# Optimization experiments

Hardware: AMD Instinct MI355X
Metric: run time of the kernel (lower is better)

The kernel has to match this reference:

```python
import jax, jax.numpy as jnp
import numpy as np

N_POINTS = 300000
N_PAIRS = 100000  # rulebook pairs per kernel offset
K_OFFSETS = 27    # 3x3x3 kernel
C_IN, C_OUT = 32, 64
GROUPS = 8
EPS = 1e-5
NEG_SLOPE = 0.01


def setup_inputs() -> dict:
    key = jax.random.key(0)
    k1, k2, k3, k4 = jax.random.split(key, 4)
    feats = jax.random.normal(k1, (N_POINTS, C_IN), dtype=jnp.float32)
    weight = jax.random.normal(k2, (K_OFFSETS, C_IN, C_OUT), dtype=jnp.float32) * (1.0 / np.sqrt(C_IN * K_OFFSETS))
    gamma = jnp.ones((C_OUT,), dtype=jnp.float32)
    beta = jnp.zeros((C_OUT,), dtype=jnp.float32)
    in_idx = jax.random.randint(k3, (K_OFFSETS, N_PAIRS), 0, N_POINTS, dtype=jnp.int64)
    out_idx = jax.random.randint(k4, (K_OFFSETS, N_PAIRS), 0, N_POINTS, dtype=jnp.int64)
    return {"feats": feats, "weight": weight, "gamma": gamma, "beta": beta,
            "in_idx": in_idx, "out_idx": out_idx}


def reference(feats, weight, gamma, beta, in_idx, out_idx):
    # Sparse 3D conv via rulebook: gather -> per-offset matmul -> scatter-add
    gathered = feats[in_idx]                       # [K, P, C_in]
    y = jnp.einsum('kpi,kio->kpo', gathered, weight)  # [K, P, C_out]
    out = jnp.zeros((feats.shape[0], weight.shape[2]), feats.dtype)
    out = out.at[out_idx.reshape(-1)].add(y.reshape(-1, weight.shape[2]))
    # GroupNorm(8, C_out): stats over all points and channels within each group
    N, C = out.shape
    xg = out.reshape(N, GROUPS, C // GROUPS)
    mean = jnp.mean(xg, axis=(0, 2), keepdims=True)
    var = jnp.var(xg, axis=(0, 2), keepdims=True)
    xn = ((xg - mean) * jax.lax.rsqrt(var + EPS)).reshape(N, C)
    xn = xn * gamma + beta
    # LeakyReLU (default negative_slope = 0.01)
    return jnp.where(xn >= 0, xn, NEG_SLOPE * xn)
```

## Files before the change

kernel.cpp:

```cpp
#include <hip/hip_runtime.h>

#define NPTS   300000
#define NPAIRS 100000
#define KOFF   27
#define CIN    32
#define COUT   64
#define NGROUP 8
#define EPSV   1e-5f
#define SLOPE  0.01f

#define PAIRS_PER_BLOCK 256
#define BLOCKS_PER_K ((NPAIRS + PAIRS_PER_BLOCK - 1) / PAIRS_PER_BLOCK)

__global__ __launch_bounds__(256) void zero_kernel(float4* __restrict__ out4, int n4,
                                                   float* __restrict__ stats) {
    int i = blockIdx.x * blockDim.x + threadIdx.x;
    if (i < n4) out4[i] = make_float4(0.f, 0.f, 0.f, 0.f);
    if (blockIdx.x == 0 && threadIdx.x < 16) stats[threadIdx.x] = 0.f;
}

__global__ __launch_bounds__(256) void conv_kernel(
    const float* __restrict__ feats, const float* __restrict__ weight,
    const int* __restrict__ in_idx, const int* __restrict__ out_idx,
    float* __restrict__ out)
{
    const int lane = threadIdx.x & 63;
    const int wave = threadIdx.x >> 6;
    const int k     = blockIdx.x / BLOCKS_PER_K;
    const int pair0 = (blockIdx.x % BLOCKS_PER_K) * PAIRS_PER_BLOCK;

    float w[CIN];
    const float* wk = weight + k * (CIN * COUT) + lane;
#pragma unroll
    for (int i = 0; i < CIN; ++i) w[i] = wk[i * COUT];

    const int per_wave = PAIRS_PER_BLOCK / 4;
    int p    = pair0 + wave * per_wave;
    int pend = p + per_wave;
    if (pend > NPAIRS) pend = NPAIRS;
    if (p >= pend) return;

    const int* ii = in_idx  + k * NPAIRS;
    const int* oi = out_idx + k * NPAIRS;

    int rin0 = __builtin_amdgcn_readfirstlane(ii[p]);
    const float* f0 = feats + (size_t)rin0 * CIN;
    float a[CIN];
#pragma unroll
    for (int i = 0; i < CIN; ++i) a[i] = f0[i];

    for (; p + 1 < pend; ++p) {
        int rin1 = __builtin_amdgcn_readfirstlane(ii[p + 1]);
        const float* f1 = feats + (size_t)rin1 * CIN;
        float b[CIN];
#pragma unroll
        for (int i = 0; i < CIN; ++i) b[i] = f1[i];

        int rout = __builtin_amdgcn_readfirstlane(oi[p]);
        float acc0 = 0.f, acc1 = 0.f;
#pragma unroll
        for (int i = 0; i < CIN; i += 2) {
            acc0 = fmaf(a[i],     w[i],     acc0);
            acc1 = fmaf(a[i + 1], w[i + 1], acc1);
        }
        atomicAdd(out + (size_t)rout * COUT + lane, acc0 + acc1);

#pragma unroll
        for (int i = 0; i < CIN; ++i) a[i] = b[i];
    }
    {
        int rout = __builtin_amdgcn_readfirstlane(oi[p]);
        float acc0 = 0.f, acc1 = 0.f;
#pragma unroll
        for (int i = 0; i < CIN; i += 2) {
            acc0 = fmaf(a[i],     w[i],     acc0);
            acc1 = fmaf(a[i + 1], w[i + 1], acc1);
        }
        atomicAdd(out + (size_t)rout * COUT + lane, acc0 + acc1);
    }
}

__global__ __launch_bounds__(256) void stats_kernel(const float4* __restrict__ out4,
                                                    float* __restrict__ stats) {
    const int tid  = blockIdx.x * 256 + threadIdx.x;
    const int ntid = gridDim.x * 256;
    const int n4   = NPTS * COUT / 4;

    float s = 0.f, ss = 0.f;
    for (int i = tid; i < n4; i += ntid) {
        float4 v = out4[i];
        s  += v.x + v.y + v.z + v.w;
        ss += v.x * v.x + v.y * v.y + v.z * v.z + v.w * v.w;
    }
    s  += __shfl_xor(s,  1, 64);  ss += __shfl_xor(ss,  1, 64);
    s  += __shfl_xor(s, 16, 64);  ss += __shfl_xor(ss, 16, 64);
    s  += __shfl_xor(s, 32, 64);  ss += __shfl_xor(ss, 32, 64);

    __shared__ float sm_s[4][NGROUP];
    __shared__ float sm_ss[4][NGROUP];
    const int lane = threadIdx.x & 63;
    const int wv   = threadIdx.x >> 6;
    if (lane < 16 && (lane & 1) == 0) {
        sm_s [wv][lane >> 1] = s;
        sm_ss[wv][lane >> 1] = ss;
    }
    __syncthreads();
    if (threadIdx.x < NGROUP) {
        float ts = 0.f, tss = 0.f;
#pragma unroll
        for (int wvi = 0; wvi < 4; ++wvi) { ts += sm_s[wvi][threadIdx.x]; tss += sm_ss[wvi][threadIdx.x]; }
        atomicAdd(stats + threadIdx.x,          ts);
        atomicAdd(stats + NGROUP + threadIdx.x, tss);
    }
}

__global__ __launch_bounds__(256) void norm_kernel(float4* __restrict__ out4, int n4,
                                                   const float* __restrict__ stats,
                                                   const float* __restrict__ gamma,
                                                   const float* __restrict__ beta) {
    int i = blockIdx.x * blockDim.x + threadIdx.x;
    if (i >= n4) return;
    int c0 = (i & 15) * 4;
    int g  = c0 >> 3;
    const float cnt = (float)NPTS * (COUT / NGROUP);
    float mean = stats[g] / cnt;
    float var  = stats[8 + g] / cnt - mean * mean;
    float inv  = rsqrtf(var + EPSV);
    float4 v  = out4[i];
    float4 ga = *(const float4*)(gamma + c0);
    float4 be = *(const float4*)(beta  + c0);
    float x;
    x = (v.x - mean) * inv * ga.x + be.x; v.x = x >= 0.f ? x : SLOPE * x;
    x = (v.y - mean) * inv * ga.y + be.y; v.y = x >= 0.f ? x : SLOPE * x;
    x = (v.z - mean) * inv * ga.z + be.z; v.z = x >= 0.f ? x : SLOPE * x;
    x = (v.w - mean) * inv * ga.w + be.w; v.w = x >= 0.f ? x : SLOPE * x;
    out4[i] = v;
}

extern "C" void kernel_launch(void* const* d_in, const int* in_sizes, int n_in,
                              void* d_out, int out_size, void* d_ws, size_t ws_size,
                              hipStream_t stream) {
    const float* feats  = (const float*)d_in[0];
    const float* weight = (const float*)d_in[1];
    const float* gamma  = (const float*)d_in[2];
    const float* beta   = (const float*)d_in[3];
    const int*   in_idx = (const int*)d_in[4];
    const int*   out_idx= (const int*)d_in[5];
    float* out   = (float*)d_out;
    float* stats = (float*)d_ws;

    int n4 = out_size / 4;
    int zb = (n4 + 255) / 256;

    zero_kernel<<<zb, 256, 0, stream>>>((float4*)out, n4, stats);
    conv_kernel<<<KOFF * BLOCKS_PER_K, 256, 0, stream>>>(feats, weight, in_idx, out_idx, out);
    stats_kernel<<<2048, 256, 0, stream>>>((const float4*)out, stats);
    norm_kernel<<<zb, 256, 0, stream>>>((float4*)out, n4, stats, gamma, beta);
}
```

Before: 769.5 us.

## Bin rulebook pairs by output row and accumulate in shared memory

Adds a counting sort of all rulebook pairs into segments keyed by kernel offset and 256-row output bin (histogram, single-block scan, scatter). A new conv kernel then handles one output bin per block, accumulating into a 64KB LDS tile with shared atomics and writing each row once. This removes the global zeroing pass and the global atomics. The cost is extra preprocessing passes, a serial one-block scan over about 32K segments, and low occupancy from 576 threads and 64KB LDS per block. The fallback path is also simplified to drop its software prefetch.

```diff
diff --git a/kernel.cpp b/kernel.cpp
--- a/kernel.cpp
+++ b/kernel.cpp
@@ -8,6 +8,136 @@
 #define NGROUP 8
 #define EPSV   1e-5f
 #define SLOPE  0.01f
+
+#define NTOT   (KOFF * NPAIRS)
+#define BINSZ  256
+#define NBIN   ((NPTS + BINSZ - 1) / BINSZ)
+#define NSEG   (KOFF * NBIN)
+#define CONV_THREADS 576
+
+#define WS_INTS_NEEDED (16 + 3 * NSEG + NTOT)
+
+__global__ __launch_bounds__(256) void zero_meta_kernel(int* __restrict__ segCount,
+                                                        float* __restrict__ stats) {
+    int i = blockIdx.x * 256 + threadIdx.x;
+    if (i < NSEG) segCount[i] = 0;
+    if (i < 16) stats[i] = 0.f;
+}
+
+__global__ __launch_bounds__(256) void hist_kernel(const int* __restrict__ out_idx,
+                                                   int* __restrict__ segCount) {
+    int g = blockIdx.x * 256 + threadIdx.x;
+    if (g >= NTOT) return;
+    int rout = out_idx[g];
+    int key = (g / NPAIRS) * NBIN + (rout >> 8);
+    atomicAdd(&segCount[key], 1);
+}
+
+__global__ __launch_bounds__(1024) void scan_kernel(const int* __restrict__ cnt,
+                                                    int* __restrict__ start,
+                                                    int* __restrict__ cursor) {
+    __shared__ int part[1024];
+    const int t = threadIdx.x;
+    const int per = (NSEG + 1023) / 1024;
+    int lo = t * per;
+    int hi = lo + per; if (hi > NSEG) hi = NSEG;
+    int s = 0;
+    for (int i = lo; i < hi && i >= 0; ++i) s += cnt[i];
+    part[t] = s;
+    __syncthreads();
+    for (int off = 1; off < 1024; off <<= 1) {
+        int v = (t >= off) ? part[t - off] : 0;
+        __syncthreads();
+        part[t] += v;
+        __syncthreads();
+    }
+    int run = (t == 0) ? 0 : part[t - 1];
+    for (int i = lo; i < hi && i >= 0; ++i) {
+        start[i] = run; cursor[i] = run;
+        run += cnt[i];
+    }
+}
+
+__global__ __launch_bounds__(256) void scatter_kernel(const int* __restrict__ out_idx,
+                                                      const int* __restrict__ in_idx,
+                                                      int* __restrict__ segCursor,
+                                                      int* __restrict__ sorted) {
+    int g = blockIdx.x * 256 + threadIdx.x;
+    if (g >= NTOT) return;
+    int rout = out_idx[g];
+    int rin  = in_idx[g];
+    int key = (g / NPAIRS) * NBIN + (rout >> 8);
+    int pos = atomicAdd(&segCursor[key], 1);
+    sorted[pos] = ((rout & (BINSZ - 1)) << 19) | rin;
+}
+
+__global__ __launch_bounds__(CONV_THREADS) void conv_binned_kernel(
+    const float* __restrict__ feats, const float* __restrict__ weight,
+    const int* __restrict__ sorted, const int* __restrict__ segStart,
+    const int* __restrict__ segCount, float* __restrict__ out)
+{
+    __shared__ float accS[BINSZ * COUT];
+    const int bin  = blockIdx.x;
+    const int lane = threadIdx.x & 63;
+    const int wv   = threadIdx.x >> 6;
+
+    for (int i = threadIdx.x; i < BINSZ * COUT; i += CONV_THREADS) accS[i] = 0.f;
+    __syncthreads();
+
+#pragma unroll
+    for (int kk = 0; kk < 3; ++kk) {
+        const int k = wv * 3 + kk;
+        const int s = k * NBIN + bin;
+        const int st  = segStart[s];
+        const int len = segCount[s];
+        if (len <= 0) continue;
+
+        float w[CIN];
+        const float* wk = weight + k * (CIN * COUT) + lane;
+#pragma unroll
+        for (int i = 0; i < CIN; ++i) w[i] = wk[i * COUT];
+
+        auto loadrow = [&](int idx, float* R) -> int {
+            int e = __builtin_amdgcn_readfirstlane(sorted[idx]);
+            const float* f = feats + (size_t)(e & 0x7FFFF) * CIN;
+#pragma unroll
+            for (int i = 0; i < CIN; ++i) R[i] = f[i];
+            return e >> 19;
+        };
+        auto compute = [&](const float* R, int rl) {
+            float a0 = 0.f, a1 = 0.f;
+#pragma unroll
+            for (int i = 0; i < CIN; i += 2) {
+                a0 = fmaf(R[i],     w[i],     a0);
+                a1 = fmaf(R[i + 1], w[i + 1], a1);
+            }
+            atomicAdd(&accS[rl * COUT + lane], a0 + a1);
+        };
+
+        const int pend = st + len;
+        float A[CIN], B[CIN];
+        int rlA = loadrow(st, A);
+        if (len == 1) { compute(A, rlA); continue; }
+        int rlB = loadrow(st + 1, B);
+        int j = st;
+        while (true) {
+            compute(A, rlA);
+            if (j + 2 < pend) rlA = loadrow(j + 2, A);
+            else { compute(B, rlB); break; }
+            compute(B, rlB);
+            if (j + 3 < pend) rlB = loadrow(j + 3, B);
+            else { compute(A, rlA); break; }
+            j += 2;
+        }
+    }
+    __syncthreads();
+
+    const int base = bin << 8;
+    for (int r = wv; r < BINSZ; r += 9) {
+        int row = base + r;
+        if (row < NPTS) out[(size_t)row * COUT + lane] = accS[r * COUT + lane];
+    }
+}
 
 #define PAIRS_PER_BLOCK 256
 #define BLOCKS_PER_K ((NPAIRS + PAIRS_PER_BLOCK - 1) / PAIRS_PER_BLOCK)
@@ -38,45 +168,19 @@
     int p    = pair0 + wave * per_wave;
     int pend = p + per_wave;
     if (pend > NPAIRS) pend = NPAIRS;
-    if (p >= pend) return;
 
     const int* ii = in_idx  + k * NPAIRS;
     const int* oi = out_idx + k * NPAIRS;
 
-    int rin0 = __builtin_amdgcn_readfirstlane(ii[p]);
-    const float* f0 = feats + (size_t)rin0 * CIN;
-    float a[CIN];
-#pragma unroll
-    for (int i = 0; i < CIN; ++i) a[i] = f0[i];
-
-    for (; p + 1 < pend; ++p) {
-        int rin1 = __builtin_amdgcn_readfirstlane(ii[p + 1]);
-        const float* f1 = feats + (size_t)rin1 * CIN;
-        float b[CIN];
-#pragma unroll
-        for (int i = 0; i < CIN; ++i) b[i] = f1[i];
-
+    for (; p < pend; ++p) {
+        int rin  = __builtin_amdgcn_readfirstlane(ii[p]);
         int rout = __builtin_amdgcn_readfirstlane(oi[p]);
-        float acc0 = 0.f, acc1 = 0.f;
-#pragma unroll
-        for (int i = 0; i < CIN; i += 2) {
-            acc0 = fmaf(a[i],     w[i],     acc0);
-            acc1 = fmaf(a[i + 1], w[i + 1], acc1);
-        }
-        atomicAdd(out + (size_t)rout * COUT + lane, acc0 + acc1);
-
-#pragma unroll
-        for (int i = 0; i < CIN; ++i) a[i] = b[i];
-    }
-    {
-        int rout = __builtin_amdgcn_readfirstlane(oi[p]);
-        float acc0 = 0.f, acc1 = 0.f;
-#pragma unroll
-        for (int i = 0; i < CIN; i += 2) {
-            acc0 = fmaf(a[i],     w[i],     acc0);
-            acc1 = fmaf(a[i + 1], w[i + 1], acc1);
-        }
-        atomicAdd(out + (size_t)rout * COUT + lane, acc0 + acc1);
+        const float* frow = feats + (size_t)rin * CIN;
+        float acc = 0.f;
+#pragma unroll
+        for (int i = 0; i < CIN; ++i)
+            acc = fmaf(frow[i], w[i], acc);
+        atomicAdd(out + (size_t)rout * COUT + lane, acc);
     }
 }
 
@@ -147,13 +251,31 @@
     const int*   in_idx = (const int*)d_in[4];
     const int*   out_idx= (const int*)d_in[5];
     float* out   = (float*)d_out;
-    float* stats = (float*)d_ws;
 
     int n4 = out_size / 4;
     int zb = (n4 + 255) / 256;
 
-    zero_kernel<<<zb, 256, 0, stream>>>((float4*)out, n4, stats);
-    conv_kernel<<<KOFF * BLOCKS_PER_K, 256, 0, stream>>>(feats, weight, in_idx, out_idx, out);
-    stats_kernel<<<2048, 256, 0, stream>>>((const float4*)out, stats);
-    norm_kernel<<<zb, 256, 0, stream>>>((float4*)out, n4, stats, gamma, beta);
-}
+    if (ws_size >= (size_t)WS_INTS_NEEDED * 4) {
+        float* stats    = (float*)d_ws;
+        int* segCount   = (int*)d_ws + 16;
+        int* segStart   = segCount + NSEG;
+        int* segCursor  = segStart + NSEG;
+        int* sorted     = segCursor + NSEG;
+
+        int pb = (NTOT + 255) / 256;
+        zero_meta_kernel<<<(NSEG + 255) / 256, 256, 0, stream>>>(segCount, stats);
+        hist_kernel<<<pb, 256, 0, stream>>>(out_idx, segCount);
+        scan_kernel<<<1, 1024, 0, stream>>>(segCount, segStart, segCursor);
+        scatter_kernel<<<pb, 256, 0, stream>>>(out_idx, in_idx, segCursor, sorted);
+        conv_binned_kernel<<<NBIN, CONV_THREADS, 0, stream>>>(feats, weight, sorted,
+                                                              segStart, segCount, out);
+        stats_kernel<<<2048, 256, 0, stream>>>((const float4*)out, stats);
+        norm_kernel<<<zb, 256, 0, stream>>>((float4*)out, n4, stats, gamma, beta);
+    } else {
+        float* stats = (float*)d_ws;
+        zero_kernel<<<zb, 256, 0, stream>>>((float4*)out, n4, stats);
+        conv_kernel<<<KOFF * BLOCKS_PER_K, 256, 0, stream>>>(feats, weight, in_idx, out_idx, out);
+        stats_kernel<<<2048, 256, 0, stream>>>((const float4*)out, stats);
+        norm_kernel<<<zb, 256, 0, stream>>>((float4*)out, n4, stats, gamma, beta);
+    }
+}
```

New measurement: 1.494 ms. +94.1%, slower.
